# Kernel optimization log

Hardware: AMD Instinct MI355X
Metric: run time of the kernel (lower is better)

Reference implementation:

```python
import jax, jax.numpy as jnp
import numpy as np

B, L, D = 4, 2048, 2048
H, KVH = 16, 4
HD = D // H            # 128
G = H // KVH           # GQA group size
K_SEL = L // 4         # top_k_ratio = 0.25 -> 512
MAX_SEQ = 8192
THETA = 10000.0
SCALE = HD ** -0.5
NEG = -1e9


def _rope_tables(dim, max_len, theta):
    inv = 1.0 / theta ** (jnp.arange(0, dim, 2, dtype=jnp.float32) / dim)  # (dim/2,)
    ang = jnp.arange(max_len, dtype=jnp.float32)[:, None] * inv[None, :]   # (max_len, dim/2)
    return jnp.cos(ang), jnp.sin(ang)


def _apply_rope_pos(x, cos, sin, pos):
    # x: (B, h, K, HD), pos: (B, K) int positions
    c = cos[pos][:, None]  # (B,1,K,HD/2)
    s = sin[pos][:, None]
    x1, x2 = jnp.split(x, 2, axis=-1)
    return jnp.concatenate([x1 * c - x2 * s, x1 * s + x2 * c], axis=-1)


def setup_inputs() -> dict:
    key = jax.random.key(0)
    ks = jax.random.split(key, 8)
    std = 0.02
    x   = jax.random.normal(ks[0], (B, L, D), dtype=jnp.float32)
    Wq  = jax.random.normal(ks[1], (D, D), dtype=jnp.float32) * std
    Wkv = jax.random.normal(ks[2], (D, 2 * KVH * HD), dtype=jnp.float32) * std
    Wo  = jax.random.normal(ks[3], (D, D), dtype=jnp.float32) * std
    W1  = jax.random.normal(ks[4], (D, D // 4), dtype=jnp.float32) * std
    b1  = jnp.zeros((D // 4,), dtype=jnp.float32)
    W2  = jax.random.normal(ks[5], (D // 4, 1), dtype=jnp.float32) * std
    b2  = jnp.zeros((1,), dtype=jnp.float32)
    return {"x": x, "Wq": Wq, "Wkv": Wkv, "Wo": Wo,
            "W1": W1, "b1": b1, "W2": W2, "b2": b2}


def reference(x, Wq, Wkv, Wo, W1, b1, W2, b2):
    Bx, Lx, Dx = x.shape
    # 1. learned per-token importance scores
    imp = (jax.nn.gelu(x @ W1 + b1, approximate=False) @ W2 + b2)[..., 0]  # (B,L)
    # 2. top-k token selection, sorted to keep original order
    _, idx = jax.lax.top_k(imp, K_SEL)
    idx = jnp.sort(idx, axis=-1)                                           # (B,K)
    x_sel = jnp.take_along_axis(x, idx[..., None], axis=1)                 # (B,K,D)
    # 3. fused KV projection on the selected subset (GQA)
    kv = x_sel @ Wkv
    k, v = jnp.split(kv, 2, axis=-1)
    k = k.reshape(Bx, K_SEL, KVH, HD).transpose(0, 2, 1, 3)                # (B,KVH,K,HD)
    v = v.reshape(Bx, K_SEL, KVH, HD).transpose(0, 2, 1, 3)
    # 4. RoPE with original positions for K, contiguous positions for Q
    cos, sin = _rope_tables(HD, MAX_SEQ, THETA)
    k = _apply_rope_pos(k, cos, sin, idx)
    q = (x @ Wq).reshape(Bx, Lx, H, HD).transpose(0, 2, 1, 3)              # (B,H,L,HD)
    qpos = jnp.broadcast_to(jnp.arange(Lx)[None, :], (Bx, Lx))
    q = _apply_rope_pos(q, cos, sin, qpos)
    # 5. GQA head expansion + attention over gathered keys
    k = jnp.repeat(k, G, axis=1)                                           # (B,H,K,HD)
    v = jnp.repeat(v, G, axis=1)
    scores = jnp.einsum('bhld,bhkd->bhlk', q, k) * SCALE                   # (B,H,L,K)
    # causal mask on original key positions
    causal = idx[:, None, None, :] > jnp.arange(Lx)[None, None, :, None]
    scores = jnp.where(causal, NEG, scores)
    attn = jax.nn.softmax(scores, axis=-1)
    # 6. importance soft gating (gradient path into the scorer)
    gate = jax.nn.sigmoid(jnp.take_along_axis(imp, idx, axis=1))           # (B,K)
    attn = attn * gate[:, None, None, :]
    out = jnp.einsum('bhlk,bhkd->bhld', attn, v)                           # (B,H,L,HD)
    out = out.transpose(0, 2, 1, 3).reshape(Bx, Lx, Dx)
    return out @ Wo
```

## Files before the change

### kernel.cpp

```cpp
#include <hip/hip_runtime.h>
#include <math.h>

typedef unsigned short u16;
typedef __attribute__((ext_vector_type(8))) short short8;
typedef __attribute__((ext_vector_type(4))) float f32x4;

__device__ __forceinline__ float bf2f(u16 u) {
  return __uint_as_float(((unsigned)u) << 16);
}
__device__ __forceinline__ u16 f2bf(float f) {
  unsigned u = __float_as_uint(f);
  return (u16)((u + 0x7fffu + ((u >> 16) & 1u)) >> 16);
}

__device__ __forceinline__ void gload_lds16(const u16* g, u16* l) {
  __builtin_amdgcn_global_load_lds((const __attribute__((address_space(1))) unsigned int*)g,
                                   (__attribute__((address_space(3))) unsigned int*)l, 16, 0, 0);
}

__device__ __forceinline__ void stage_tile(const u16* __restrict__ gbase, int ldg,
                                           u16* lds, int w, int lane) {
  #pragma unroll
  for (int i = 0; i < 4; ++i) {
    int c = w * 4 + i;
    const u16* g = gbase + (size_t)(c * 8 + (lane >> 3)) * ldg + (lane & 7) * 8;
    gload_lds16(g, lds + c * 512);
  }
}

__global__ __launch_bounds__(256) void cvt_x_kernel(const float* __restrict__ x,
                                                    u16* __restrict__ xb,
                                                    u16* __restrict__ xlo) {
  size_t base = ((size_t)blockIdx.x * 256 + threadIdx.x) * 8;
  short8 hi, lo;
  #pragma unroll
  for (int i = 0; i < 8; ++i) {
    float v = x[base + i];
    u16 h = f2bf(v);
    hi[i] = (short)h;
    lo[i] = (short)f2bf(v - bf2f(h));
  }
  *(short8*)&xb[base] = hi;
  *(short8*)&xlo[base] = lo;
}

template <bool HILO>
__global__ __launch_bounds__(256) void transpose_cvt(const float* __restrict__ in,
                                                     u16* __restrict__ outH,
                                                     u16* __restrict__ outL,
                                                     int R, int C) {
  __shared__ u16 tH[64][72];
  __shared__ u16 tL[64][72];
  int rb = blockIdx.y * 64, cb = blockIdx.x * 64;
  int t = threadIdx.x;
  #pragma unroll
  for (int i = 0; i < 16; ++i) {
    int r = i * 4 + (t >> 6), c = t & 63;
    float v = in[(size_t)(rb + r) * C + cb + c];
    u16 h = f2bf(v);
    tH[r][c] = h;
    if (HILO) tL[r][c] = f2bf(v - bf2f(h));
  }
  __syncthreads();
  #pragma unroll
  for (int i = 0; i < 16; ++i) {
    int r = i * 4 + (t >> 6), c = t & 63;
    outH[(size_t)(cb + r) * R + rb + c] = tH[c][r];
    if (HILO) outL[(size_t)(cb + r) * R + rb + c] = tL[c][r];
  }
}

__global__ void ropetab_kernel(float* __restrict__ cosT, float* __restrict__ sinT) {
  int pos = blockIdx.x, i = threadIdx.x;
  float e = (float)(2 * i) * (1.0f / 128.0f);
  float inv = powf(10000.0f, -e);
  float ang = (float)pos * inv;
  cosT[pos * 64 + i] = cosf(ang);
  sinT[pos * 64 + i] = sinf(ang);
}

template <bool BF16OUT>
__global__ __launch_bounds__(512, 2) void gemm256(const u16* __restrict__ A,
                                                  const u16* __restrict__ BT,
                                                  float* __restrict__ Cf,
                                                  u16* __restrict__ Cb,
                                                  int M, int N, int K) {
  __shared__ __align__(1024) u16 smem[65536];
  const int bm = blockIdx.x * 256, bn = blockIdx.y * 256;
  const int t = threadIdx.x, lane = t & 63, w = t >> 6;
  const int ll = lane & 15, lh = lane >> 4;
  const int wr = w >> 2, wc = w & 3;
  const int NT = K >> 6;

  const int tt0 = t, tt1 = t + 512;
  const int r0 = tt0 >> 2, r1 = tt1 >> 2;
  const int c0 = (((tt0 & 3) ^ ((tt0 >> 3) & 3)) << 3);
  const int c1 = (((tt1 & 3) ^ ((tt1 >> 3) & 3)) << 3);
  const size_t aoff0 = (size_t)(bm + r0) * K + c0;
  const size_t aoff1 = (size_t)(bm + r1) * K + c1;
  const size_t boff0 = (size_t)(bn + r0) * K + c0;
  const size_t boff1 = (size_t)(bn + r1) * K + c1;

  const int swz = ((lh ^ ((ll >> 1) & 3)) << 3);
  const int arow = (wr * 128 + ll) * 32 + swz;
  const int brow = (wc * 64 + ll) * 32 + swz;

  f32x4 acc[8][4];
  #pragma unroll
  for (int mi = 0; mi < 8; ++mi)
    #pragma unroll
    for (int ni = 0; ni < 4; ++ni) acc[mi][ni] = f32x4{0.f, 0.f, 0.f, 0.f};

  short8 aq[8], bq[2];

#define G_STAGE(base, o0, o1, lds) \
  gload_lds16((base) + (o0), (lds) + w * 512); \
  gload_lds16((base) + (o1), (lds) + 4096 + w * 512)
#define RD_A(Sa, ks) \
  _Pragma("unroll") for (int mi = 0; mi < 8; ++mi) aq[mi] = *(const short8*)&(Sa)[(ks)*8192 + arow + mi * 512]
#define RD_B(Sb, ks, nh) \
  _Pragma("unroll") for (int n2 = 0; n2 < 2; ++n2) bq[n2] = *(const short8*)&(Sb)[(ks)*8192 + brow + ((nh)*2 + n2) * 512]
#define DO_MFMA(nh) \
  __builtin_amdgcn_s_setprio(1); \
  _Pragma("unroll") for (int mi = 0; mi < 8; ++mi) \
    _Pragma("unroll") for (int n2 = 0; n2 < 2; ++n2) \
      acc[mi][(nh)*2 + n2] = __builtin_amdgcn_mfma_f32_16x16x32_bf16(aq[mi], bq[n2], acc[mi][(nh)*2 + n2], 0, 0, 0); \
  __builtin_amdgcn_s_setprio(0)
#define VMW(n) asm volatile("s_waitcnt vmcnt(" #n ")" ::: "memory")

  G_STAGE(A, aoff0, aoff1, smem);
  G_STAGE(BT, boff0, boff1, smem + 16384);
  G_STAGE(A, aoff0 + 32, aoff1 + 32, smem + 8192);
  G_STAGE(BT, boff0 + 32, boff1 + 32, smem + 16384 + 8192);

  for (int kt = 0; kt < NT - 1; ++kt) {
    const int cur = kt & 1;
    u16* Sa = smem + cur * 32768;
    u16* Sb = Sa + 16384;
    u16* Pa = smem + (cur ^ 1) * 32768;
    u16* Pb = Pa + 16384;
    const size_t kg = (size_t)(kt + 1) * 64;
    VMW(4);
    __builtin_amdgcn_s_barrier();
    G_STAGE(A, aoff0 + kg, aoff1 + kg, Pa);
    RD_A(Sa, 0);
    RD_B(Sb, 0, 0);
    DO_MFMA(0);
    G_STAGE(BT, boff0 + kg, boff1 + kg, Pb);
    RD_B(Sb, 0, 1);
    DO_MFMA(1);
    VMW(4);
    __builtin_amdgcn_s_barrier();
    G_STAGE(A, aoff0 + kg + 32, aoff1 + kg + 32, Pa + 8192);
    RD_A(Sa, 1);
    RD_B(Sb, 1, 0);
    DO_MFMA(0);
    G_STAGE(BT, boff0 + kg + 32, boff1 + kg + 32, Pb + 8192);
    RD_B(Sb, 1, 1);
    DO_MFMA(1);
  }
  {
    const int cur = (NT - 1) & 1;
    u16* Sa = smem + cur * 32768;
    u16* Sb = Sa + 16384;
    VMW(4);
    __builtin_amdgcn_s_barrier();
    RD_A(Sa, 0); RD_B(Sb, 0, 0); DO_MFMA(0);
    RD_B(Sb, 0, 1); DO_MFMA(1);
    VMW(0);
    __builtin_amdgcn_s_barrier();
    RD_A(Sa, 1); RD_B(Sb, 1, 0); DO_MFMA(0);
    RD_B(Sb, 1, 1); DO_MFMA(1);
  }

  #pragma unroll
  for (int mi = 0; mi < 8; ++mi)
    #pragma unroll
    for (int ni = 0; ni < 4; ++ni)
      #pragma unroll
      for (int r = 0; r < 4; ++r) {
        int row = bm + wr * 128 + mi * 16 + lh * 4 + r;
        int col = bn + wc * 64 + ni * 16 + ll;
        float v = acc[mi][ni][r];
        if (BF16OUT) Cb[(size_t)row * N + col] = f2bf(v);
        else Cf[(size_t)row * N + col] = v;
      }
#undef G_STAGE
#undef RD_A
#undef RD_B
#undef DO_MFMA
#undef VMW
}

__global__ __launch_bounds__(256) void gemm_bt_gather(const u16* __restrict__ A,
                                                      const u16* __restrict__ BT,
                                                      const int* __restrict__ rowidx,
                                                      float* __restrict__ Cpart,
                                                      int M, int N, int K) {
  constexpr int BK = 64;
  __shared__ u16 As[128][BK + 8];
  __shared__ u16 Bs[128][BK + 8];
  const int bm = blockIdx.x * 128, bn = blockIdx.y * 128;
  const int kz = blockIdx.z;
  const int t = threadIdx.x, lane = t & 63, w = t >> 6;
  const int lh = lane >> 4, ll = lane & 15;
  const int wm = (w >> 1) * 64, wn = (w & 1) * 64;
  f32x4 acc[4][4];
  #pragma unroll
  for (int mt = 0; mt < 4; ++mt)
    #pragma unroll
    for (int nt = 0; nt < 4; ++nt) acc[mt][nt] = f32x4{0.f, 0.f, 0.f, 0.f};

  const int k0 = kz * (K / 2), k1 = k0 + K / 2;
  for (int kb = k0; kb < k1; kb += BK) {
    __syncthreads();
    #pragma unroll
    for (int i = 0; i < 4; ++i) {
      int e = t + i * 256;
      int row = e >> 3, c8 = e & 7;
      int arow = rowidx[bm + row];
      *(short8*)&As[row][c8 * 8] = *(const short8*)&A[(size_t)arow * K + kb + c8 * 8];
      *(short8*)&Bs[row][c8 * 8] = *(const short8*)&BT[(size_t)(bn + row) * K + kb + c8 * 8];
    }
    __syncthreads();
    #pragma unroll
    for (int ks = 0; ks < 2; ++ks) {
      short8 a[4], b[4];
      #pragma unroll
      for (int mt = 0; mt < 4; ++mt) a[mt] = *(const short8*)&As[wm + mt * 16 + ll][ks * 32 + lh * 8];
      #pragma unroll
      for (int nt = 0; nt < 4; ++nt) b[nt] = *(const short8*)&Bs[wn + nt * 16 + ll][ks * 32 + lh * 8];
      #pragma unroll
      for (int mt = 0; mt < 4; ++mt)
        #pragma unroll
        for (int nt = 0; nt < 4; ++nt)
          acc[mt][nt] = __builtin_amdgcn_mfma_f32_16x16x32_bf16(a[mt], b[nt], acc[mt][nt], 0, 0, 0);
    }
  }
  float* C = Cpart + (size_t)kz * M * N;
  #pragma unroll
  for (int mt = 0; mt < 4; ++mt)
    #pragma unroll
    for (int nt = 0; nt < 4; ++nt)
      #pragma unroll
      for (int r = 0; r < 4; ++r) {
        int row = bm + wm + mt * 16 + lh * 4 + r;
        int col = bn + wn + nt * 16 + ll;
        C[(size_t)row * N + col] = acc[mt][nt][r];
      }
}

__global__ __launch_bounds__(256) void gemm_scorer(const u16* __restrict__ Ahi,
                                                   const u16* __restrict__ Alo,
                                                   const u16* __restrict__ Bhi,
                                                   const u16* __restrict__ Blo,
                                                   float* __restrict__ Cpart,
                                                   int M, int N, int K) {
  __shared__ __align__(1024) u16 smem[4 * 128 * 64];
  u16* AsH = smem;
  u16* AsL = smem + 128 * 64;
  u16* BsH = smem + 2 * 128 * 64;
  u16* BsL = smem + 3 * 128 * 64;
  const int bm = blockIdx.x * 128, bn = blockIdx.y * 128;
  const int kz = blockIdx.z;
  const int t = threadIdx.x, lane = t & 63, w = t >> 6;
  const int lh = lane >> 4, ll = lane & 15;
  const int wm = (w >> 1) * 64, wn = (w & 1) * 64;
  f32x4 acc[4][4];
  #pragma unroll
  for (int mt = 0; mt < 4; ++mt)
    #pragma unroll
    for (int nt = 0; nt < 4; ++nt) acc[mt][nt] = f32x4{0.f, 0.f, 0.f, 0.f};

  const int k0 = kz * (K / 2), k1 = k0 + K / 2;
  for (int kb = k0; kb < k1; kb += 64) {
    __syncthreads();
    stage_tile(Ahi + (size_t)bm * K + kb, K, AsH, w, lane);
    stage_tile(Alo + (size_t)bm * K + kb, K, AsL, w, lane);
    stage_tile(Bhi + (size_t)bn * K + kb, K, BsH, w, lane);
    stage_tile(Blo + (size_t)bn * K + kb, K, BsL, w, lane);
    __syncthreads();
    #pragma unroll
    for (int ks = 0; ks < 2; ++ks) {
      short8 ah[4], al[4], bh[4], bl[4];
      #pragma unroll
      for (int mt = 0; mt < 4; ++mt) {
        int o = (wm + mt * 16 + ll) * 64 + ks * 32 + lh * 8;
        ah[mt] = *(const short8*)&AsH[o];
        al[mt] = *(const short8*)&AsL[o];
      }
      #pragma unroll
      for (int nt = 0; nt < 4; ++nt) {
        int o = (wn + nt * 16 + ll) * 64 + ks * 32 + lh * 8;
        bh[nt] = *(const short8*)&BsH[o];
        bl[nt] = *(const short8*)&BsL[o];
      }
      #pragma unroll
      for (int mt = 0; mt < 4; ++mt)
        #pragma unroll
        for (int nt = 0; nt < 4; ++nt) {
          acc[mt][nt] = __builtin_amdgcn_mfma_f32_16x16x32_bf16(ah[mt], bh[nt], acc[mt][nt], 0, 0, 0);
          acc[mt][nt] = __builtin_amdgcn_mfma_f32_16x16x32_bf16(ah[mt], bl[nt], acc[mt][nt], 0, 0, 0);
          acc[mt][nt] = __builtin_amdgcn_mfma_f32_16x16x32_bf16(al[mt], bh[nt], acc[mt][nt], 0, 0, 0);
        }
    }
  }
  float* C = Cpart + (size_t)kz * M * N;
  #pragma unroll
  for (int mt = 0; mt < 4; ++mt)
    #pragma unroll
    for (int nt = 0; nt < 4; ++nt)
      #pragma unroll
      for (int r = 0; r < 4; ++r) {
        int row = bm + wm + mt * 16 + lh * 4 + r;
        int col = bn + wn + nt * 16 + ll;
        C[(size_t)row * N + col] = acc[mt][nt][r];
      }
}

__global__ __launch_bounds__(256) void scorer_finish(const float* __restrict__ hg,
                                                     const float* __restrict__ b1,
                                                     const float* __restrict__ W2,
                                                     const float* __restrict__ b2,
                                                     float* __restrict__ imp) {
  int tok = blockIdx.x * 4 + (threadIdx.x >> 6);
  int lane = threadIdx.x & 63;
  const float* h0 = hg + (size_t)tok * 512;
  const float* h1 = hg + (size_t)8192 * 512 + (size_t)tok * 512;
  float s = 0.f;
  #pragma unroll
  for (int i = 0; i < 8; ++i) {
    int c = lane + i * 64;
    float v = h0[c] + h1[c] + b1[c];
    v = 0.5f * v * (1.0f + erff(v * 0.70710678118654752f));
    s += v * W2[c];
  }
  #pragma unroll
  for (int off = 32; off; off >>= 1) s += __shfl_xor(s, off, 64);
  if (lane == 0) imp[tok] = s + b2[0];
}

__global__ __launch_bounds__(1024) void topk_kernel(const float* __restrict__ imp,
                                                    int* __restrict__ idx_sel,
                                                    int* __restrict__ sel_rows,
                                                    float* __restrict__ gatev) {
  __shared__ float v[2048];
  __shared__ int ix[2048];
  __shared__ int ids[512];
  int b = blockIdx.x, t = threadIdx.x;
  for (int i = t; i < 2048; i += 1024) { v[i] = imp[b * 2048 + i]; ix[i] = i; }
  __syncthreads();
  for (int k = 2; k <= 2048; k <<= 1)
    for (int j = k >> 1; j > 0; j >>= 1) {
      int i = ((t & ~(j - 1)) << 1) | (t & (j - 1));
      int l2 = i | j;
      bool dir = ((i & k) == 0);
      float vi = v[i], vl = v[l2];
      int xi = ix[i], xl = ix[l2];
      bool g = (vi < vl) || (vi == vl && xi > xl);
      if (g == dir) { v[i] = vl; v[l2] = vi; ix[i] = xl; ix[l2] = xi; }
      __syncthreads();
    }
  if (t < 512) ids[t] = ix[t];
  __syncthreads();
  for (int k = 2; k <= 512; k <<= 1)
    for (int j = k >> 1; j > 0; j >>= 1) {
      if (t < 256) {
        int i = ((t & ~(j - 1)) << 1) | (t & (j - 1));
        int l2 = i | j;
        bool dir = ((i & k) == 0);
        int ai = ids[i], al = ids[l2];
        if ((ai > al) == dir) { ids[i] = al; ids[l2] = ai; }
      }
      __syncthreads();
    }
  if (t < 512) {
    int id = ids[t];
    idx_sel[b * 512 + t] = id;
    sel_rows[b * 512 + t] = b * 2048 + id;
    float g = imp[b * 2048 + id];
    gatev[b * 512 + t] = 1.0f / (1.0f + __expf(-g));
  }
}

__global__ __launch_bounds__(256) void rope_k2(const float* __restrict__ part,
                                               const int* __restrict__ idx_sel,
                                               const float* __restrict__ cosT,
                                               const float* __restrict__ sinT,
                                               u16* __restrict__ Kb) {
  int gid = blockIdx.x * 256 + threadIdx.x;
  int i = gid & 63;
  int s = (gid >> 6) & 511;
  int kvh = (gid >> 15) & 3;
  int b = gid >> 17;
  size_t src = (size_t)(b * 512 + s) * 1024 + kvh * 128 + i;
  float k1 = part[src] + part[src + 2097152];
  float k2 = part[src + 64] + part[src + 64 + 2097152];
  int pos = idx_sel[b * 512 + s];
  float c = cosT[pos * 64 + i], sn = sinT[pos * 64 + i];
  size_t dst = (size_t)((b * 4 + kvh) * 512 + s) * 128 + i;
  Kb[dst] = f2bf(k1 * c - k2 * sn);
  Kb[dst + 64] = f2bf(k1 * sn + k2 * c);
}

__global__ __launch_bounds__(256) void vtrans2(const float* __restrict__ part,
                                               const float* __restrict__ gatev,
                                               u16* __restrict__ VT) {
  int gid = blockIdx.x * 256 + threadIdx.x;
  int s = gid & 511;
  int d = (gid >> 9) & 127;
  int kvh = (gid >> 16) & 3;
  int b = gid >> 18;
  size_t src = (size_t)(b * 512 + s) * 1024 + 512 + kvh * 128 + d;
  float v = part[src] + part[src + 2097152];
  VT[(size_t)((b * 4 + kvh) * 128 + d) * 512 + s] = f2bf(v * gatev[b * 512 + s]);
}

__global__ __launch_bounds__(512) void attn_kernel(const u16* __restrict__ Qb,
                                                   const u16* __restrict__ Kb,
                                                   const u16* __restrict__ VTb,
                                                   const int* __restrict__ idxp,
                                                   const float* __restrict__ cosT,
                                                   const float* __restrict__ sinT,
                                                   u16* __restrict__ Ob) {
  __shared__ u16 KPs[8704];
  __shared__ u16 Vs[128][76];

  const int qt = blockIdx.x, h = blockIdx.y, b = blockIdx.z;
  const int kvh = h >> 2;
  const int t = threadIdx.x, lane = t & 63, w = t >> 6;
  const int lh = lane >> 4, ll = lane & 15;
  const int q0 = qt * 128;
  const float SCALE_LOG2E = 0.12753102331f;

  int NT = 8;
  if (idxp[b * 512] <= q0) {
    NT = 1;
    while (NT < 8 && idxp[b * 512 + NT * 64] <= q0 + 127) ++NT;
  }

  const int lrow = q0 + w * 16 + ll;
  short8 aq[4];
  #pragma unroll
  for (int ks = 0; ks < 4; ++ks)
    aq[ks] = *(const short8*)&Qb[(size_t)(b * 2048 + lrow) * 2048 + h * 128 + ks * 32 + lh * 8];
  {
    const float* cp = cosT + (size_t)lrow * 64 + lh * 8;
    const float* sp = sinT + (size_t)lrow * 64 + lh * 8;
    short8 n0, n1, n2, n3;
    #pragma unroll
    for (int j = 0; j < 8; ++j) {
      float cA = cp[j], sA = sp[j], cB = cp[32 + j], sB = sp[32 + j];
      float x0 = bf2f((u16)aq[0][j]), x2 = bf2f((u16)aq[2][j]);
      float x1 = bf2f((u16)aq[1][j]), x3 = bf2f((u16)aq[3][j]);
      n0[j] = (short)f2bf(x0 * cA - x2 * sA);
      n2[j] = (short)f2bf(x0 * sA + x2 * cA);
      n1[j] = (short)f2bf(x1 * cB - x3 * sB);
      n3[j] = (short)f2bf(x1 * sB + x3 * cB);
    }
    aq[0] = n0; aq[1] = n1; aq[2] = n2; aq[3] = n3;
  }

  float m[4], lden[4];
  f32x4 O[8];
  #pragma unroll
  for (int r = 0; r < 4; ++r) { m[r] = -INFINITY; lden[r] = 0.f; }
  #pragma unroll
  for (int dt = 0; dt < 8; ++dt) O[dt] = f32x4{0.f, 0.f, 0.f, 0.f};

  const int krow = t >> 4, kc8 = t & 15;
  const int vrow = t >> 3, vc8 = t & 7;

  for (int kt = 0; kt < NT; ++kt) {
    const int tmax = idxp[b * 512 + kt * 64 + 63];
    const bool nomask = (tmax <= q0 + w * 16);

    __syncthreads();
    #pragma unroll
    for (int i = 0; i < 2; ++i) {
      int kr = krow + i * 32;
      *(short8*)&KPs[kr * 136 + kc8 * 8] =
          *(const short8*)&Kb[(size_t)((b * 4 + kvh) * 512 + kt * 64 + kr) * 128 + kc8 * 8];
      int vr = vrow + i * 64;
      *(short8*)&Vs[vr][vc8 * 8] =
          *(const short8*)&VTb[(size_t)((b * 4 + kvh) * 128 + vr) * 512 + kt * 64 + vc8 * 8];
    }
    __syncthreads();

    f32x4 S[4];
    #pragma unroll
    for (int nt = 0; nt < 4; ++nt) S[nt] = f32x4{0.f, 0.f, 0.f, 0.f};
    #pragma unroll
    for (int nt = 0; nt < 4; ++nt)
      #pragma unroll
      for (int ks = 0; ks < 4; ++ks) {
        short8 bk = *(const short8*)&KPs[(nt * 16 + ll) * 136 + ks * 32 + lh * 8];
        S[nt] = __builtin_amdgcn_mfma_f32_16x16x32_bf16(aq[ks], bk, S[nt], 0, 0, 0);
      }
    __syncthreads();

    float p[4][4], lmax[4];
    #pragma unroll
    for (int r = 0; r < 4; ++r) lmax[r] = -INFINITY;
    if (nomask) {
      #pragma unroll
      for (int nt = 0; nt < 4; ++nt)
        #pragma unroll
        for (int r = 0; r < 4; ++r) {
          float s = S[nt][r] * SCALE_LOG2E;
          p[nt][r] = s;
          lmax[r] = fmaxf(lmax[r], s);
        }
    } else {
      #pragma unroll
      for (int nt = 0; nt < 4; ++nt) {
        int kpos = idxp[b * 512 + kt * 64 + nt * 16 + ll];
        #pragma unroll
        for (int r = 0; r < 4; ++r) {
          int row = q0 + w * 16 + lh * 4 + r;
          float s = S[nt][r] * SCALE_LOG2E;
          if (kpos > row) s = -1e9f;
          p[nt][r] = s;
          lmax[r] = fmaxf(lmax[r], s);
        }
      }
    }
    #pragma unroll
    for (int off = 8; off; off >>= 1)
      #pragma unroll
      for (int r = 0; r < 4; ++r) lmax[r] = fmaxf(lmax[r], __shfl_xor(lmax[r], off, 64));

    bool need = false;
    #pragma unroll
    for (int r = 0; r < 4; ++r) need = need || (lmax[r] > m[r] + 8.0f);
    if (__any(need)) {
      #pragma unroll
      for (int r = 0; r < 4; ++r) {
        float mnew = fmaxf(m[r], lmax[r]);
        float alpha = exp2f(m[r] - mnew);
        m[r] = mnew;
        lden[r] *= alpha;
        #pragma unroll
        for (int dt = 0; dt < 8; ++dt) O[dt][r] *= alpha;
      }
    }

    float rs[4] = {0.f, 0.f, 0.f, 0.f};
    #pragma unroll
    for (int nt = 0; nt < 4; ++nt)
      #pragma unroll
      for (int r = 0; r < 4; ++r) {
        float e = exp2f(p[nt][r] - m[r]);
        p[nt][r] = e;
        rs[r] += e;
      }
    #pragma unroll
    for (int off = 8; off; off >>= 1)
      #pragma unroll
      for (int r = 0; r < 4; ++r) rs[r] += __shfl_xor(rs[r], off, 64);
    #pragma unroll
    for (int r = 0; r < 4; ++r) lden[r] += rs[r];

    #pragma unroll
    for (int nt = 0; nt < 4; ++nt)
      #pragma unroll
      for (int r = 0; r < 4; r += 2) {
        unsigned pk;
        asm("v_cvt_pk_bf16_f32 %0, %1, %2" : "=v"(pk) : "v"(p[nt][r]), "v"(p[nt][r + 1]));
        KPs[w * 1088 + (lh * 4 + r) * 68 + nt * 16 + ll] = (u16)pk;
        KPs[w * 1088 + (lh * 4 + r + 1) * 68 + nt * 16 + ll] = (u16)(pk >> 16);
      }
    #pragma unroll
    for (int ks = 0; ks < 2; ++ks) {
      short8 pa = *(const short8*)&KPs[w * 1088 + ll * 68 + ks * 32 + lh * 8];
      #pragma unroll
      for (int dt = 0; dt < 8; ++dt) {
        short8 vb = *(const short8*)&Vs[dt * 16 + ll][ks * 32 + lh * 8];
        O[dt] = __builtin_amdgcn_mfma_f32_16x16x32_bf16(pa, vb, O[dt], 0, 0, 0);
      }
    }
  }

  #pragma unroll
  for (int dt = 0; dt < 8; ++dt)
    #pragma unroll
    for (int r = 0; r < 4; ++r) {
      int row = q0 + w * 16 + lh * 4 + r;
      int col = h * 128 + dt * 16 + ll;
      Ob[(size_t)(b * 2048 + row) * 2048 + col] = f2bf(O[dt][r] / lden[r]);
    }
}

extern "C" void kernel_launch(void* const* d_in, const int* in_sizes, int n_in,
                              void* d_out, int out_size, void* d_ws, size_t ws_size,
                              hipStream_t stream) {
  const float* x = (const float*)d_in[0];
  const float* Wq = (const float*)d_in[1];
  const float* Wkv = (const float*)d_in[2];
  const float* Wo = (const float*)d_in[3];
  const float* W1 = (const float*)d_in[4];
  const float* b1 = (const float*)d_in[5];
  const float* W2 = (const float*)d_in[6];
  const float* b2 = (const float*)d_in[7];
  float* out = (float*)d_out;

  char* ws = (char*)d_ws;
  size_t off = 0;
  auto alloc = [&](size_t bytes) {
    char* p = ws + off;
    off = (off + bytes + 255) & ~(size_t)255;
    return p;
  };
  u16* xb = (u16*)alloc((size_t)8192 * 2048 * 2);
  u16* xlo = (u16*)alloc((size_t)8192 * 2048 * 2);
  u16* W1Th = (u16*)alloc((size_t)512 * 2048 * 2);
  u16* W1Tl = (u16*)alloc((size_t)512 * 2048 * 2);
  u16* WqT = (u16*)alloc((size_t)2048 * 2048 * 2);
  u16* WkvT = (u16*)alloc((size_t)1024 * 2048 * 2);
  u16* WoT = (u16*)alloc((size_t)2048 * 2048 * 2);
  float* cosT = (float*)alloc((size_t)2048 * 64 * 4);
  float* sinT = (float*)alloc((size_t)2048 * 64 * 4);
  float* hg = (float*)alloc((size_t)2 * 8192 * 512 * 4);
  float* impv = (float*)alloc((size_t)8192 * 4);
  int* idx_sel = (int*)alloc((size_t)2048 * 4);
  int* sel_rows = (int*)alloc((size_t)2048 * 4);
  float* gatev = (float*)alloc((size_t)2048 * 4);
  u16* qbuf = (u16*)alloc((size_t)8192 * 2048 * 2);
  u16* Kbuf = (u16*)alloc((size_t)4 * 4 * 512 * 128 * 2);
  u16* VTbuf = (u16*)alloc((size_t)4 * 4 * 128 * 512 * 2);
  u16* attn_out = xlo;
  float* kvpart = hg;

  cvt_x_kernel<<<8192, 256, 0, stream>>>(x, xb, xlo);
  transpose_cvt<true><<<dim3(512 / 64, 2048 / 64), 256, 0, stream>>>(W1, W1Th, W1Tl, 2048, 512);
  transpose_cvt<false><<<dim3(32, 32), 256, 0, stream>>>(Wq, WqT, nullptr, 2048, 2048);
  transpose_cvt<false><<<dim3(16, 32), 256, 0, stream>>>(Wkv, WkvT, nullptr, 2048, 1024);
  transpose_cvt<false><<<dim3(32, 32), 256, 0, stream>>>(Wo, WoT, nullptr, 2048, 2048);
  ropetab_kernel<<<2048, 64, 0, stream>>>(cosT, sinT);

  gemm_scorer<<<dim3(64, 4, 2), 256, 0, stream>>>(xb, xlo, W1Th, W1Tl, hg, 8192, 512, 2048);
  scorer_finish<<<2048, 256, 0, stream>>>(hg, b1, W2, b2, impv);
  topk_kernel<<<4, 1024, 0, stream>>>(impv, idx_sel, sel_rows, gatev);

  gemm256<true><<<dim3(32, 8), 512, 0, stream>>>(xb, WqT, nullptr, qbuf, 8192, 2048, 2048);

  gemm_bt_gather<<<dim3(16, 8, 2), 256, 0, stream>>>(xb, WkvT, sel_rows, kvpart, 2048, 1024, 2048);
  rope_k2<<<2048, 256, 0, stream>>>(kvpart, idx_sel, cosT, sinT, Kbuf);
  vtrans2<<<4096, 256, 0, stream>>>(kvpart, gatev, VTbuf);

  attn_kernel<<<dim3(16, 16, 4), 512, 0, stream>>>(qbuf, Kbuf, VTbuf, idx_sel, cosT, sinT, attn_out);

  gemm256<false><<<dim3(32, 8), 512, 0, stream>>>(attn_out, WoT, out, nullptr, 8192, 2048, 2048);
}
```

Before: 386.5 us.

## Read K/V directly from global memory in attention, drop LDS staging and barriers

The attention kernel no longer stages K and V tiles into shared memory with block-wide barriers. Each wave now reads its MFMA B-operands straight from global memory (relying on L1/L2 caching) and keeps only a small per-wave LDS buffer for the P matrix. Blocks shrink to 4 waves over 64 query rows, and each wave computes its own causal tile count. This removes synchronisation and LDS traffic and allows finer early exit per wave, at the cost of repeated uncoalesced global reads of K/V across waves.

Result: slower. 555.0 us (+43.6%).

```diff
diff --git a/kernel.cpp b/kernel.cpp
--- a/kernel.cpp
+++ b/kernel.cpp
@@ -416,30 +416,29 @@
   VT[(size_t)((b * 4 + kvh) * 128 + d) * 512 + s] = f2bf(v * gatev[b * 512 + s]);
 }
 
-__global__ __launch_bounds__(512) void attn_kernel(const u16* __restrict__ Qb,
+__global__ __launch_bounds__(256) void attn_kernel(const u16* __restrict__ Qb,
                                                    const u16* __restrict__ Kb,
                                                    const u16* __restrict__ VTb,
                                                    const int* __restrict__ idxp,
                                                    const float* __restrict__ cosT,
                                                    const float* __restrict__ sinT,
                                                    u16* __restrict__ Ob) {
-  __shared__ u16 KPs[8704];
-  __shared__ u16 Vs[128][76];
+  __shared__ u16 Ps[4][16][68];
 
   const int qt = blockIdx.x, h = blockIdx.y, b = blockIdx.z;
   const int kvh = h >> 2;
   const int t = threadIdx.x, lane = t & 63, w = t >> 6;
   const int lh = lane >> 4, ll = lane & 15;
-  const int q0 = qt * 128;
+  const int q0 = qt * 64 + w * 16;
   const float SCALE_LOG2E = 0.12753102331f;
 
   int NT = 8;
   if (idxp[b * 512] <= q0) {
     NT = 1;
-    while (NT < 8 && idxp[b * 512 + NT * 64] <= q0 + 127) ++NT;
-  }
-
-  const int lrow = q0 + w * 16 + ll;
+    while (NT < 8 && idxp[b * 512 + NT * 64] <= q0 + 15) ++NT;
+  }
+
+  const int lrow = q0 + ll;
   short8 aq[4];
   #pragma unroll
   for (int ks = 0; ks < 4; ++ks)
@@ -461,6 +460,9 @@
     aq[0] = n0; aq[1] = n1; aq[2] = n2; aq[3] = n3;
   }
 
+  const u16* Kbase = Kb + (size_t)((b * 4 + kvh) * 512) * 128;
+  const u16* Vbase = VTb + (size_t)((b * 4 + kvh) * 128) * 512;
+
   float m[4], lden[4];
   f32x4 O[8];
   #pragma unroll
@@ -468,24 +470,9 @@
   #pragma unroll
   for (int dt = 0; dt < 8; ++dt) O[dt] = f32x4{0.f, 0.f, 0.f, 0.f};
 
-  const int krow = t >> 4, kc8 = t & 15;
-  const int vrow = t >> 3, vc8 = t & 7;
-
   for (int kt = 0; kt < NT; ++kt) {
     const int tmax = idxp[b * 512 + kt * 64 + 63];
-    const bool nomask = (tmax <= q0 + w * 16);
-
-    __syncthreads();
-    #pragma unroll
-    for (int i = 0; i < 2; ++i) {
-      int kr = krow + i * 32;
-      *(short8*)&KPs[kr * 136 + kc8 * 8] =
-          *(const short8*)&Kb[(size_t)((b * 4 + kvh) * 512 + kt * 64 + kr) * 128 + kc8 * 8];
-      int vr = vrow + i * 64;
-      *(short8*)&Vs[vr][vc8 * 8] =
-          *(const short8*)&VTb[(size_t)((b * 4 + kvh) * 128 + vr) * 512 + kt * 64 + vc8 * 8];
-    }
-    __syncthreads();
+    const bool nomask = (tmax <= q0);
 
     f32x4 S[4];
     #pragma unroll
@@ -494,10 +481,9 @@
     for (int nt = 0; nt < 4; ++nt)
       #pragma unroll
       for (int ks = 0; ks < 4; ++ks) {
-        short8 bk = *(const short8*)&KPs[(nt * 16 + ll) * 136 + ks * 32 + lh * 8];
+        short8 bk = *(const short8*)&Kbase[(size_t)(kt * 64 + nt * 16 + ll) * 128 + ks * 32 + lh * 8];
         S[nt] = __builtin_amdgcn_mfma_f32_16x16x32_bf16(aq[ks], bk, S[nt], 0, 0, 0);
       }
-    __syncthreads();
 
     float p[4][4], lmax[4];
     #pragma unroll
@@ -517,7 +503,7 @@
         int kpos = idxp[b * 512 + kt * 64 + nt * 16 + ll];
         #pragma unroll
         for (int r = 0; r < 4; ++r) {
-          int row = q0 + w * 16 + lh * 4 + r;
+          int row = q0 + lh * 4 + r;
           float s = S[nt][r] * SCALE_LOG2E;
           if (kpos > row) s = -1e9f;
           p[nt][r] = s;
@@ -567,15 +553,15 @@
       for (int r = 0; r < 4; r += 2) {
         unsigned pk;
         asm("v_cvt_pk_bf16_f32 %0, %1, %2" : "=v"(pk) : "v"(p[nt][r]), "v"(p[nt][r + 1]));
-        KPs[w * 1088 + (lh * 4 + r) * 68 + nt * 16 + ll] = (u16)pk;
-        KPs[w * 1088 + (lh * 4 + r + 1) * 68 + nt * 16 + ll] = (u16)(pk >> 16);
+        Ps[w][lh * 4 + r][nt * 16 + ll] = (u16)pk;
+        Ps[w][lh * 4 + r + 1][nt * 16 + ll] = (u16)(pk >> 16);
       }
     #pragma unroll
     for (int ks = 0; ks < 2; ++ks) {
-      short8 pa = *(const short8*)&KPs[w * 1088 + ll * 68 + ks * 32 + lh * 8];
+      short8 pa = *(const short8*)&Ps[w][ll][ks * 32 + lh * 8];
       #pragma unroll
       for (int dt = 0; dt < 8; ++dt) {
-        short8 vb = *(const short8*)&Vs[dt * 16 + ll][ks * 32 + lh * 8];
+        short8 vb = *(const short8*)&Vbase[(size_t)(dt * 16 + ll) * 512 + kt * 64 + ks * 32 + lh * 8];
         O[dt] = __builtin_amdgcn_mfma_f32_16x16x32_bf16(pa, vb, O[dt], 0, 0, 0);
       }
     }
@@ -585,7 +571,7 @@
   for (int dt = 0; dt < 8; ++dt)
     #pragma unroll
     for (int r = 0; r < 4; ++r) {
-      int row = q0 + w * 16 + lh * 4 + r;
+      int row = q0 + lh * 4 + r;
       int col = h * 128 + dt * 16 + ll;
       Ob[(size_t)(b * 2048 + row) * 2048 + col] = f2bf(O[dt][r] / lden[r]);
     }
@@ -648,7 +634,7 @@
   rope_k2<<<2048, 256, 0, stream>>>(kvpart, idx_sel, cosT, sinT, Kbuf);
   vtrans2<<<4096, 256, 0, stream>>>(kvpart, gatev, VTbuf);
 
-  attn_kernel<<<dim3(16, 16, 4), 512, 0, stream>>>(qbuf, Kbuf, VTbuf, idx_sel, cosT, sinT, attn_out);
+  attn_kernel<<<dim3(32, 16, 4), 256, 0, stream>>>(qbuf, Kbuf, VTbuf, idx_sel, cosT, sinT, attn_out);
 
   gemm256<false><<<dim3(32, 8), 512, 0, stream>>>(attn_out, WoT, out, nullptr, 8192, 2048, 2048);
 }
```
